# Kernel optimization log

Hardware: AMD Instinct MI355X
Metric: run time of the kernel (lower is better)

## Reference

```python
import jax, jax.numpy as jnp
import numpy as np

E = 8           # ensemble size
D_IN = 512      # input_dim (state+action)
H = 1024        # hidden size, arch=[1024, 1024]
D_OUT = 1       # output_dim (Q value)
LN_EPS = 1e-5


def setup_inputs() -> dict:
    key = jax.random.key(0)
    ks = jax.random.split(key, 8)
    s1 = 1.0 / np.sqrt(D_IN)
    s2 = 1.0 / np.sqrt(H)
    return {
        "x": jax.random.normal(ks[0], (16384, D_IN), dtype=jnp.float32),
        # stacked per-ensemble parameters: leading axis E
        "W1": jax.random.uniform(ks[1], (E, D_IN, H), jnp.float32, -s1, s1),
        "b1": jax.random.uniform(ks[2], (E, H), jnp.float32, -s1, s1),
        "g1": jnp.ones((E, H), jnp.float32),
        "be1": jnp.zeros((E, H), jnp.float32),
        "W2": jax.random.uniform(ks[3], (E, H, H), jnp.float32, -s2, s2),
        "b2": jax.random.uniform(ks[4], (E, H), jnp.float32, -s2, s2),
        "g2": jnp.ones((E, H), jnp.float32),
        "be2": jnp.zeros((E, H), jnp.float32),
        "W3": jax.random.uniform(ks[5], (E, H, D_OUT), jnp.float32, -s2, s2),
        "b3": jax.random.uniform(ks[6], (E, D_OUT), jnp.float32, -s2, s2),
    }


def _layer_norm(h, g, b):
    # h: [E, B, H]; g, b: [E, H] -> broadcast over batch
    mu = jnp.mean(h, axis=-1, keepdims=True)
    var = jnp.mean(jnp.square(h - mu), axis=-1, keepdims=True)
    return (h - mu) * jax.lax.rsqrt(var + LN_EPS) * g[:, None, :] + b[:, None, :]


def reference(x, W1, b1, g1, be1, W2, b2, g2, be2, W3, b3):
    # Layer 1: all ensemble members as one batched GEMM on shared input
    h = jnp.einsum('bd,edh->ebh', x, W1) + b1[:, None, :]       # [E, B, H]
    h = jax.nn.relu(_layer_norm(h, g1, be1))
    # Layer 2
    h = jnp.einsum('ebd,edh->ebh', h, W2) + b2[:, None, :]      # [E, B, H]
    h = jax.nn.relu(_layer_norm(h, g2, be2))
    # Head (identity head activation)
    qs = jnp.einsum('ebd,edo->ebo', h, W3) + b3[:, None, :]      # [E, B, 1]
    q = jnp.min(qs, axis=0)                                      # [B, 1]
    return (q, qs)
```

## Files before the change

kernel.cpp:

```cpp
#include <hip/hip_runtime.h>
#include <hip/hip_bf16.h>
#include <stdint.h>

#define EN    8
#define DIN   512
#define HID   1024
#define BATCH 16384
#define LN_EPS 1e-5f

#define BM 256
#define BN 128
#define BK 32

typedef __bf16   bf16x8 __attribute__((ext_vector_type(8)));
typedef float    f32x4  __attribute__((ext_vector_type(4)));
typedef uint16_t u16x8  __attribute__((ext_vector_type(8)));
typedef uint16_t u16x4  __attribute__((ext_vector_type(4)));
typedef float    fl4    __attribute__((ext_vector_type(4)));

__device__ __forceinline__ uint16_t f2bf(float f) {
  uint32_t x = __builtin_bit_cast(uint32_t, f);
  uint32_t r = (x + 0x7fffu + ((x >> 16) & 1u)) >> 16;
  return (uint16_t)r;
}
__device__ __forceinline__ float bf2f(uint16_t u) {
  return __builtin_bit_cast(float, (uint32_t)u << 16);
}

__device__ __forceinline__ void gload16(const uint16_t* g, uint16_t* lds) {
  __builtin_amdgcn_global_load_lds(
      (const __attribute__((address_space(1))) uint32_t*)g,
      (__attribute__((address_space(3))) uint32_t*)lds, 16, 0, 0);
}

__device__ __forceinline__ f32x4 MF(bf16x8 a, bf16x8 b, f32x4 c) {
  return __builtin_amdgcn_mfma_f32_16x16x32_bf16(a, b, c, 0, 0, 0);
}

__global__ __launch_bounds__(256) void cvt_bf16(const float* __restrict__ src,
                                                uint16_t* __restrict__ dst, long n) {
  long i = ((long)blockIdx.x * 256 + threadIdx.x) * 4;
  if (i >= n) return;
  fl4 v = *(const fl4*)(src + i);
  u16x4 o;
  #pragma unroll
  for (int j = 0; j < 4; ++j) o[j] = f2bf(v[j]);
  *(u16x4*)(dst + i) = o;
}

__global__ __launch_bounds__(256) void transpose_cvt(const float* __restrict__ src,
                                                     uint16_t* __restrict__ dst,
                                                     int R, int C) {
  __shared__ float tile[32][33];
  const int e = blockIdx.z;
  const int c0 = blockIdx.x * 32;
  const int r0 = blockIdx.y * 32;
  const int tx = threadIdx.x & 31, ty = threadIdx.x >> 5;
  const float* s = src + (size_t)e * R * C;
  uint16_t*    d = dst + (size_t)e * R * C;
  #pragma unroll
  for (int i = 0; i < 32; i += 8)
    tile[ty + i][tx] = s[(size_t)(r0 + ty + i) * C + (c0 + tx)];
  __syncthreads();
  #pragma unroll
  for (int i = 0; i < 32; i += 8)
    d[(size_t)(c0 + ty + i) * R + (r0 + tx)] = f2bf(tile[tx][ty + i]);
}

__global__ __launch_bounds__(512, 4) void gemm_rb(
    const uint16_t* __restrict__ A, size_t a_estride,
    const uint16_t* __restrict__ Bt,
    const float*    __restrict__ bias,
    uint16_t*       __restrict__ C,
    int M, int K) {
  __shared__ __attribute__((aligned(16))) char lds[73728];
  const int tid = threadIdx.x;
  const int bx  = blockIdx.x;
  const int e   = bx & 7;
  const int t   = bx >> 3;
  const int mt  = t >> 3;
  const int nt  = t & 7;
  const int NT  = K >> 5;

  const uint16_t* Ae = A + (size_t)e * a_estride + (size_t)(mt * BM) * K;
  const uint16_t* Be = Bt + ((size_t)e * HID + nt * BN) * K;

  const int l  = tid & 63, wid = tid >> 6;
  const int wr = wid >> 1, wc = wid & 1;
  const int fr = l & 15, kq = l >> 4;
  const int swf = (fr ^ (fr >> 2)) & 3;

  const int srow  = tid >> 2;
  const int sunit = (tid & 3) ^ ((srow ^ (srow >> 2)) & 3);
  const uint16_t* pA = Ae + (size_t)srow * K + sunit * 8;
  const uint16_t* pB = Be + (size_t)srow * K + sunit * 8;
  char* const ld_t = lds + tid * 16;

  const int aoff = (wr * 64 + fr) * 64 + ((kq ^ swf) << 4);
  const int boff = 16384 + (wc * 64 + fr) * 64 + ((kq ^ swf) << 4);

  f32x4 acc[4][4];
  #pragma unroll
  for (int i = 0; i < 4; ++i)
    #pragma unroll
    for (int j = 0; j < 4; ++j) acc[i][j] = (f32x4)0.0f;

  auto STAGE = [&](int kt) {
    char* db = ld_t + (kt % 3) * 24576;
    const uint16_t* a0 = pA + kt * BK;
    gload16(a0, (uint16_t*)db);
    gload16(a0 + (size_t)128 * K, (uint16_t*)(db + 8192));
    gload16(pB + kt * BK, (uint16_t*)(db + 16384));
  };

  STAGE(0);
  STAGE(1);
  asm volatile("s_waitcnt vmcnt(3)" ::: "memory");
  __builtin_amdgcn_s_barrier();

  for (int kt = 0; kt < NT; ++kt) {
    if (kt + 2 < NT) STAGE(kt + 2);
    const char* rb = lds + (kt % 3) * 24576;
    bf16x8 af[4], bv[4];
    #pragma unroll
    for (int mi = 0; mi < 4; ++mi) af[mi] = *(const bf16x8*)(rb + aoff + mi * 1024);
    #pragma unroll
    for (int ni = 0; ni < 4; ++ni) bv[ni] = *(const bf16x8*)(rb + boff + ni * 1024);
    __builtin_amdgcn_s_setprio(1);
    #pragma unroll
    for (int ni = 0; ni < 4; ++ni)
      #pragma unroll
      for (int mi = 0; mi < 4; ++mi)
        acc[mi][ni] = MF(af[mi], bv[ni], acc[mi][ni]);
    __builtin_amdgcn_s_setprio(0);
    if (kt + 2 < NT)      asm volatile("s_waitcnt vmcnt(3)" ::: "memory");
    else if (kt + 1 < NT) asm volatile("s_waitcnt vmcnt(0)" ::: "memory");
    if (kt + 1 < NT) __builtin_amdgcn_s_barrier();
  }

  const int col0 = nt * BN + wc * 64 + fr;
  const int row0 = mt * BM + wr * 64 + kq * 4;
  float bvv[4];
  #pragma unroll
  for (int ni = 0; ni < 4; ++ni) bvv[ni] = bias[(size_t)e * HID + col0 + ni * 16];
  #pragma unroll
  for (int mi = 0; mi < 4; ++mi) {
    #pragma unroll
    for (int i = 0; i < 4; ++i) {
      const int rg = row0 + mi * 16 + i;
      uint16_t* cp = C + ((size_t)e * M + rg) * HID + col0;
      #pragma unroll
      for (int ni = 0; ni < 4; ++ni)
        cp[ni * 16] = f2bf(acc[mi][ni][i] + bvv[ni]);
    }
  }
}

__global__ __launch_bounds__(256) void ln_relu(uint16_t* __restrict__ h,
                                               const float* __restrict__ g,
                                               const float* __restrict__ be,
                                               int kshift) {
  const int wid = threadIdx.x >> 6, l = threadIdx.x & 63;
  const long row = (long)blockIdx.x * 4 + wid;
  const int e = (int)(row >> kshift);
  uint16_t* p = h + row * HID;

  u16x8 s0 = *(const u16x8*)(p + l * 8);
  u16x8 s1 = *(const u16x8*)(p + 512 + l * 8);
  float v[16];
  #pragma unroll
  for (int j = 0; j < 8; ++j) { v[j] = bf2f(s0[j]); v[8 + j] = bf2f(s1[j]); }

  float sum = 0.f, sq = 0.f;
  #pragma unroll
  for (int j = 0; j < 16; ++j) { sum += v[j]; sq += v[j] * v[j]; }
  #pragma unroll
  for (int m = 1; m < 64; m <<= 1) {
    sum += __shfl_xor(sum, m);
    sq  += __shfl_xor(sq, m);
  }
  const float mu  = sum * (1.0f / HID);
  const float var = sq * (1.0f / HID) - mu * mu;
  const float rs  = rsqrtf(var + LN_EPS);

  const float* gp = g  + (size_t)e * HID;
  const float* bp = be + (size_t)e * HID;
  u16x8 o0, o1;
  #pragma unroll
  for (int j = 0; j < 8; ++j) {
    const int c0 = l * 8 + j, c1 = 512 + l * 8 + j;
    float x0 = (v[j]     - mu) * rs * gp[c0] + bp[c0];
    float x1 = (v[8 + j] - mu) * rs * gp[c1] + bp[c1];
    o0[j] = f2bf(fmaxf(x0, 0.f));
    o1[j] = f2bf(fmaxf(x1, 0.f));
  }
  *(u16x8*)(p + l * 8) = o0;
  *(u16x8*)(p + 512 + l * 8) = o1;
}

__global__ __launch_bounds__(256) void ln_head(const uint16_t* __restrict__ h,
                                               const float* __restrict__ g,
                                               const float* __restrict__ be,
                                               const float* __restrict__ W3,
                                               const float* __restrict__ b3,
                                               float* __restrict__ out,
                                               int b0, int CB) {
  __shared__ float qsh[EN];
  const int wv = threadIdx.x >> 6, l = threadIdx.x & 63;
  const long b = blockIdx.x;
  #pragma unroll
  for (int ee = 0; ee < 2; ++ee) {
    const int e = wv + ee * 4;
    const uint16_t* p = h + ((size_t)e * CB + b) * HID;
    u16x8 s0 = *(const u16x8*)(p + l * 8);
    u16x8 s1 = *(const u16x8*)(p + 512 + l * 8);
    float v[16];
    #pragma unroll
    for (int j = 0; j < 8; ++j) { v[j] = bf2f(s0[j]); v[8 + j] = bf2f(s1[j]); }
    float sum = 0.f, sq = 0.f;
    #pragma unroll
    for (int j = 0; j < 16; ++j) { sum += v[j]; sq += v[j] * v[j]; }
    #pragma unroll
    for (int m = 1; m < 64; m <<= 1) {
      sum += __shfl_xor(sum, m);
      sq  += __shfl_xor(sq, m);
    }
    const float mu  = sum * (1.0f / HID);
    const float var = sq * (1.0f / HID) - mu * mu;
    const float rs  = rsqrtf(var + LN_EPS);
    const float* gp = g  + (size_t)e * HID;
    const float* bp = be + (size_t)e * HID;
    const float* w  = W3 + (size_t)e * HID;
    float dot = 0.f;
    #pragma unroll
    for (int j = 0; j < 8; ++j) {
      const int c0 = l * 8 + j, c1 = 512 + l * 8 + j;
      float x0 = fmaxf((v[j]     - mu) * rs * gp[c0] + bp[c0], 0.f);
      float x1 = fmaxf((v[8 + j] - mu) * rs * gp[c1] + bp[c1], 0.f);
      dot += x0 * w[c0] + x1 * w[c1];
    }
    #pragma unroll
    for (int m = 1; m < 64; m <<= 1) dot += __shfl_xor(dot, m);
    if (l == 0) {
      const float qe = dot + b3[e];
      qsh[e] = qe;
      out[BATCH + (size_t)e * BATCH + b0 + b] = qe;
    }
  }
  __syncthreads();
  if (threadIdx.x == 0) {
    float m = qsh[0];
    #pragma unroll
    for (int i = 1; i < EN; ++i) m = fminf(m, qsh[i]);
    out[b0 + b] = m;
  }
}

extern "C" void kernel_launch(void* const* d_in, const int* in_sizes, int n_in,
                              void* d_out, int out_size, void* d_ws, size_t ws_size,
                              hipStream_t stream) {
  const float* x   = (const float*)d_in[0];
  const float* W1  = (const float*)d_in[1];
  const float* b1  = (const float*)d_in[2];
  const float* g1  = (const float*)d_in[3];
  const float* be1 = (const float*)d_in[4];
  const float* W2  = (const float*)d_in[5];
  const float* b2  = (const float*)d_in[6];
  const float* g2  = (const float*)d_in[7];
  const float* be2 = (const float*)d_in[8];
  const float* W3  = (const float*)d_in[9];
  const float* b3  = (const float*)d_in[10];
  float* out = (float*)d_out;

  char* ws = (char*)d_ws;
  uint16_t* xb  = (uint16_t*)ws; ws += (size_t)BATCH * DIN * 2;
  uint16_t* w1t = (uint16_t*)ws; ws += (size_t)EN * DIN * HID * 2;
  uint16_t* w2t = (uint16_t*)ws; ws += (size_t)EN * HID * HID * 2;
  size_t fixed = (size_t)(ws - (char*)d_ws);

  size_t avail = (ws_size > fixed) ? (ws_size - fixed) : 0;
  const size_t per_row = 2ULL * EN * HID * 2ULL;
  int CB = BATCH;
  while (CB > 256 && (size_t)CB * per_row > avail) CB >>= 1;
  const int nchunks = BATCH / CB;
  const int kshift = __builtin_ctz(CB);

  uint16_t* h1 = (uint16_t*)ws; ws += (size_t)EN * CB * HID * 2;
  uint16_t* h2 = (uint16_t*)ws;

  cvt_bf16<<<(BATCH * DIN / 4 + 255) / 256, 256, 0, stream>>>(x, xb, (long)BATCH * DIN);
  transpose_cvt<<<dim3(HID / 32, DIN / 32, EN), 256, 0, stream>>>(W1, w1t, DIN, HID);
  transpose_cvt<<<dim3(HID / 32, HID / 32, EN), 256, 0, stream>>>(W2, w2t, HID, HID);

  const int gblocks = (CB / BM) * (HID / BN) * EN;

  for (int c = 0; c < nchunks; ++c) {
    const int b0 = c * CB;
    gemm_rb<<<gblocks, 512, 0, stream>>>(xb + (size_t)b0 * DIN, (size_t)0,
                                         w1t, b1, h1, CB, DIN);
    ln_relu<<<(EN * CB) / 4, 256, 0, stream>>>(h1, g1, be1, kshift);
    gemm_rb<<<gblocks, 512, 0, stream>>>(h1, (size_t)CB * HID,
                                         w2t, b2, h2, CB, HID);
    ln_head<<<CB, 256, 0, stream>>>(h2, g2, be2, W3, b3, out, b0, CB);
  }
}
```

Before: 677.5 us.

## Rewrite GEMM as 256x256 tile, 4-wave kernel with double-buffered LDS

Replaces the 256x128x32 GEMM, which used 8 waves per block and a triple-buffered LDS pipeline, with a 256x256x64 tile computed by 4 waves. Each wave owns a 128x128 sub-tile of 64 accumulators. LDS is double-buffered at 128 KB, with register prefetch of the next k-slice's fragments and an 8-way XOR swizzle. The goal is higher arithmetic intensity per LDS and global byte and fewer barriers. In exchange, each CU runs only one block, which risks register pressure and spills from 256 accumulator VGPRs and gives less latency hiding.

```diff
diff --git a/kernel.cpp b/kernel.cpp
--- a/kernel.cpp
+++ b/kernel.cpp
@@ -8,10 +8,6 @@
 #define BATCH 16384
 #define LN_EPS 1e-5f
 
-#define BM 256
-#define BN 128
-#define BK 32
-
 typedef __bf16   bf16x8 __attribute__((ext_vector_type(8)));
 typedef float    f32x4  __attribute__((ext_vector_type(4)));
 typedef uint16_t u16x8  __attribute__((ext_vector_type(8)));
@@ -27,15 +23,17 @@
   return __builtin_bit_cast(float, (uint32_t)u << 16);
 }
 
-__device__ __forceinline__ void gload16(const uint16_t* g, uint16_t* lds) {
+__device__ __forceinline__ void gload16(const uint16_t* g, char* lds_d) {
   __builtin_amdgcn_global_load_lds(
       (const __attribute__((address_space(1))) uint32_t*)g,
-      (__attribute__((address_space(3))) uint32_t*)lds, 16, 0, 0);
+      (__attribute__((address_space(3))) uint32_t*)lds_d, 16, 0, 0);
 }
 
 __device__ __forceinline__ f32x4 MF(bf16x8 a, bf16x8 b, f32x4 c) {
   return __builtin_amdgcn_mfma_f32_16x16x32_bf16(a, b, c, 0, 0, 0);
 }
+
+#define SB0() __builtin_amdgcn_sched_barrier(0)
 
 __global__ __launch_bounds__(256) void cvt_bf16(const float* __restrict__ src,
                                                 uint16_t* __restrict__ dst, long n) {
@@ -67,91 +65,118 @@
     d[(size_t)(c0 + ty + i) * R + (r0 + tx)] = f2bf(tile[tx][ty + i]);
 }
 
-__global__ __launch_bounds__(512, 4) void gemm_rb(
+__global__ __launch_bounds__(256, 1) void gemm4w(
     const uint16_t* __restrict__ A, size_t a_estride,
     const uint16_t* __restrict__ Bt,
     const float*    __restrict__ bias,
     uint16_t*       __restrict__ C,
     int M, int K) {
-  __shared__ __attribute__((aligned(16))) char lds[73728];
+  __shared__ __attribute__((aligned(16))) char lds[131072];
   const int tid = threadIdx.x;
   const int bx  = blockIdx.x;
   const int e   = bx & 7;
   const int t   = bx >> 3;
-  const int mt  = t >> 3;
-  const int nt  = t & 7;
-  const int NT  = K >> 5;
-
-  const uint16_t* Ae = A + (size_t)e * a_estride + (size_t)(mt * BM) * K;
-  const uint16_t* Be = Bt + ((size_t)e * HID + nt * BN) * K;
+  const int mt  = t >> 2;
+  const int nt  = t & 3;
+  const int NT  = K >> 6;
+
+  const uint16_t* Ae = A + (size_t)e * a_estride + (size_t)(mt * 256) * K;
+  const uint16_t* Be = Bt + ((size_t)e * HID + nt * 256) * K;
 
   const int l  = tid & 63, wid = tid >> 6;
   const int wr = wid >> 1, wc = wid & 1;
-  const int fr = l & 15, kq = l >> 4;
-  const int swf = (fr ^ (fr >> 2)) & 3;
-
-  const int srow  = tid >> 2;
-  const int sunit = (tid & 3) ^ ((srow ^ (srow >> 2)) & 3);
-  const uint16_t* pA = Ae + (size_t)srow * K + sunit * 8;
-  const uint16_t* pB = Be + (size_t)srow * K + sunit * 8;
-  char* const ld_t = lds + tid * 16;
-
-  const int aoff = (wr * 64 + fr) * 64 + ((kq ^ swf) << 4);
-  const int boff = 16384 + (wc * 64 + fr) * 64 + ((kq ^ swf) << 4);
-
-  f32x4 acc[4][4];
-  #pragma unroll
-  for (int i = 0; i < 4; ++i)
-    #pragma unroll
-    for (int j = 0; j < 4; ++j) acc[i][j] = (f32x4)0.0f;
+  const int fr = l & 15, kq = l >> 4, f7 = fr & 7;
+
+  const int r8 = l >> 3;
+  const int su = (l & 7) ^ r8;
+  const uint16_t* pA = Ae + (size_t)(wid * 8 + r8) * K + su * 8;
+  const uint16_t* pB = Be + (size_t)(wid * 8 + r8) * K + su * 8;
+  char* const dst0 = lds + tid * 16;
+
+  const int rdA0 = (wr * 128 + fr) * 128 + ((kq ^ f7) << 4);
+  const int rdB0 = 32768 + (wc * 128 + fr) * 128 + ((kq ^ f7) << 4);
+
+  f32x4 acc[8][8];
+  #pragma unroll
+  for (int i = 0; i < 8; ++i)
+    #pragma unroll
+    for (int j = 0; j < 8; ++j) acc[i][j] = (f32x4)0.0f;
 
   auto STAGE = [&](int kt) {
-    char* db = ld_t + (kt % 3) * 24576;
-    const uint16_t* a0 = pA + kt * BK;
-    gload16(a0, (uint16_t*)db);
-    gload16(a0 + (size_t)128 * K, (uint16_t*)(db + 8192));
-    gload16(pB + kt * BK, (uint16_t*)(db + 16384));
+    char* db = dst0 + ((kt & 1) << 16);
+    const uint16_t* sa = pA + kt * 64;
+    const uint16_t* sb = pB + kt * 64;
+    #pragma unroll
+    for (int j = 0; j < 8; ++j) gload16(sa + (size_t)(j * 32) * K, db + j * 4096);
+    #pragma unroll
+    for (int j = 0; j < 8; ++j) gload16(sb + (size_t)(j * 32) * K, db + 32768 + j * 4096);
   };
 
   STAGE(0);
-  STAGE(1);
-  asm volatile("s_waitcnt vmcnt(3)" ::: "memory");
+  asm volatile("s_waitcnt vmcnt(0)");
+  SB0();
   __builtin_amdgcn_s_barrier();
+  SB0();
+
+  bf16x8 a0[8], b0[8], a1[8], b1[8];
+  {
+    const char* rb = lds;
+    #pragma unroll
+    for (int i = 0; i < 8; ++i) {
+      a0[i] = *(const bf16x8*)(rb + rdA0 + i * 2048);
+      b0[i] = *(const bf16x8*)(rb + rdB0 + i * 2048);
+    }
+  }
 
   for (int kt = 0; kt < NT; ++kt) {
-    if (kt + 2 < NT) STAGE(kt + 2);
-    const char* rb = lds + (kt % 3) * 24576;
-    bf16x8 af[4], bv[4];
-    #pragma unroll
-    for (int mi = 0; mi < 4; ++mi) af[mi] = *(const bf16x8*)(rb + aoff + mi * 1024);
-    #pragma unroll
-    for (int ni = 0; ni < 4; ++ni) bv[ni] = *(const bf16x8*)(rb + boff + ni * 1024);
-    __builtin_amdgcn_s_setprio(1);
-    #pragma unroll
-    for (int ni = 0; ni < 4; ++ni)
+    const char* rb = lds + ((kt & 1) << 16);
+    const char* rq = lds + (((kt + 1) & 1) << 16);
+    if (kt + 1 < NT) STAGE(kt + 1);
+    #pragma unroll
+    for (int mi = 0; mi < 8; ++mi) {
+      a1[mi] = *(const bf16x8*)(rb + ((rdA0 + mi * 2048) ^ 64));
+      b1[mi] = *(const bf16x8*)(rb + ((rdB0 + mi * 2048) ^ 64));
+      __builtin_amdgcn_s_setprio(1);
       #pragma unroll
-      for (int mi = 0; mi < 4; ++mi)
-        acc[mi][ni] = MF(af[mi], bv[ni], acc[mi][ni]);
-    __builtin_amdgcn_s_setprio(0);
-    if (kt + 2 < NT)      asm volatile("s_waitcnt vmcnt(3)" ::: "memory");
-    else if (kt + 1 < NT) asm volatile("s_waitcnt vmcnt(0)" ::: "memory");
-    if (kt + 1 < NT) __builtin_amdgcn_s_barrier();
-  }
-
-  const int col0 = nt * BN + wc * 64 + fr;
-  const int row0 = mt * BM + wr * 64 + kq * 4;
-  float bvv[4];
-  #pragma unroll
-  for (int ni = 0; ni < 4; ++ni) bvv[ni] = bias[(size_t)e * HID + col0 + ni * 16];
-  #pragma unroll
-  for (int mi = 0; mi < 4; ++mi) {
+      for (int ni = 0; ni < 8; ++ni)
+        acc[mi][ni] = MF(a0[mi], b0[ni], acc[mi][ni]);
+      __builtin_amdgcn_s_setprio(0);
+    }
+    #pragma unroll
+    for (int mi = 0; mi < 8; ++mi) {
+      __builtin_amdgcn_s_setprio(1);
+      #pragma unroll
+      for (int ni = 0; ni < 8; ++ni)
+        acc[mi][ni] = MF(a1[mi], b1[ni], acc[mi][ni]);
+      __builtin_amdgcn_s_setprio(0);
+    }
+    if (kt + 1 < NT) {
+      asm volatile("s_waitcnt vmcnt(0)");
+      SB0();
+      __builtin_amdgcn_s_barrier();
+      SB0();
+      #pragma unroll
+      for (int i = 0; i < 8; ++i) {
+        a0[i] = *(const bf16x8*)(rq + rdA0 + i * 2048);
+        b0[i] = *(const bf16x8*)(rq + rdB0 + i * 2048);
+      }
+    }
+  }
+
+  const int col0 = nt * 256 + wc * 128 + fr;
+  const int row0 = mt * 256 + wr * 128 + kq * 4;
+  float bv[8];
+  #pragma unroll
+  for (int ni = 0; ni < 8; ++ni) bv[ni] = bias[(size_t)e * HID + col0 + ni * 16];
+  #pragma unroll
+  for (int mi = 0; mi < 8; ++mi) {
     #pragma unroll
     for (int i = 0; i < 4; ++i) {
       const int rg = row0 + mi * 16 + i;
       uint16_t* cp = C + ((size_t)e * M + rg) * HID + col0;
       #pragma unroll
-      for (int ni = 0; ni < 4; ++ni)
-        cp[ni * 16] = f2bf(acc[mi][ni][i] + bvv[ni]);
+      for (int ni = 0; ni < 8; ++ni)
+        cp[ni * 16] = f2bf(acc[mi][ni][i] + bv[ni]);
     }
   }
 }
@@ -292,15 +317,15 @@
   transpose_cvt<<<dim3(HID / 32, DIN / 32, EN), 256, 0, stream>>>(W1, w1t, DIN, HID);
   transpose_cvt<<<dim3(HID / 32, HID / 32, EN), 256, 0, stream>>>(W2, w2t, HID, HID);
 
-  const int gblocks = (CB / BM) * (HID / BN) * EN;
+  const int gblocks = (CB / 256) * (HID / 256) * EN;
 
   for (int c = 0; c < nchunks; ++c) {
     const int b0 = c * CB;
-    gemm_rb<<<gblocks, 512, 0, stream>>>(xb + (size_t)b0 * DIN, (size_t)0,
-                                         w1t, b1, h1, CB, DIN);
+    gemm4w<<<gblocks, 256, 0, stream>>>(xb + (size_t)b0 * DIN, (size_t)0,
+                                        w1t, b1, h1, CB, DIN);
     ln_relu<<<(EN * CB) / 4, 256, 0, stream>>>(h1, g1, be1, kshift);
-    gemm_rb<<<gblocks, 512, 0, stream>>>(h1, (size_t)CB * HID,
-                                         w2t, b2, h2, CB, HID);
+    gemm4w<<<gblocks, 256, 0, stream>>>(h1, (size_t)CB * HID,
+                                        w2t, b2, h2, CB, HID);
     ln_head<<<CB, 256, 0, stream>>>(h2, g2, be2, W3, b3, out, b0, CB);
   }
 }
```

Result: faster. 659.8 us (median of 4 runs) (-2.6%).

## Use 256-thread GEMM blocks with 128x64 per-warp tiles and new LDS swizzle

Applied to the files above, without the earlier changes.

The GEMM kernel drops from 512 to 256 threads per block while keeping the 256x128 block tile, so each wave now computes a 128x64 sub-tile with 8x4 MFMA accumulators. This doubles register-level reuse of the B fragments per LDS read. The LDS layout and swizzle change to 128-byte rows with a new XOR pattern, and each thread issues six async global-to-LDS loads per stage. The s_setprio hints are removed, and the doubled accumulator set raises register pressure, lowering occupancy to two blocks per CU.

```diff
diff --git a/kernel.cpp b/kernel.cpp
--- a/kernel.cpp
+++ b/kernel.cpp
@@ -8,10 +8,6 @@
 #define BATCH 16384
 #define LN_EPS 1e-5f
 
-#define BM 256
-#define BN 128
-#define BK 32
-
 typedef __bf16   bf16x8 __attribute__((ext_vector_type(8)));
 typedef float    f32x4  __attribute__((ext_vector_type(4)));
 typedef uint16_t u16x8  __attribute__((ext_vector_type(8)));
@@ -27,10 +23,10 @@
   return __builtin_bit_cast(float, (uint32_t)u << 16);
 }
 
-__device__ __forceinline__ void gload16(const uint16_t* g, uint16_t* lds) {
+__device__ __forceinline__ void gload16(const uint16_t* g, char* lds_d) {
   __builtin_amdgcn_global_load_lds(
       (const __attribute__((address_space(1))) uint32_t*)g,
-      (__attribute__((address_space(3))) uint32_t*)lds, 16, 0, 0);
+      (__attribute__((address_space(3))) uint32_t*)lds_d, 16, 0, 0);
 }
 
 __device__ __forceinline__ f32x4 MF(bf16x8 a, bf16x8 b, f32x4 c) {
@@ -67,7 +63,7 @@
     d[(size_t)(c0 + ty + i) * R + (r0 + tx)] = f2bf(tile[tx][ty + i]);
 }
 
-__global__ __launch_bounds__(512, 4) void gemm_rb(
+__global__ __launch_bounds__(256, 2) void gemm_t2(
     const uint16_t* __restrict__ A, size_t a_estride,
     const uint16_t* __restrict__ Bt,
     const float*    __restrict__ bias,
@@ -82,69 +78,76 @@
   const int nt  = t & 7;
   const int NT  = K >> 5;
 
-  const uint16_t* Ae = A + (size_t)e * a_estride + (size_t)(mt * BM) * K;
-  const uint16_t* Be = Bt + ((size_t)e * HID + nt * BN) * K;
+  const uint16_t* Ae = A + (size_t)e * a_estride + (size_t)(mt * 256) * K;
+  const uint16_t* Be = Bt + ((size_t)e * HID + nt * 128) * K;
 
   const int l  = tid & 63, wid = tid >> 6;
   const int wr = wid >> 1, wc = wid & 1;
   const int fr = l & 15, kq = l >> 4;
-  const int swf = (fr ^ (fr >> 2)) & 3;
-
-  const int srow  = tid >> 2;
-  const int sunit = (tid & 3) ^ ((srow ^ (srow >> 2)) & 3);
-  const uint16_t* pA = Ae + (size_t)srow * K + sunit * 8;
-  const uint16_t* pB = Be + (size_t)srow * K + sunit * 8;
-  char* const ld_t = lds + tid * 16;
-
-  const int aoff = (wr * 64 + fr) * 64 + ((kq ^ swf) << 4);
-  const int boff = 16384 + (wc * 64 + fr) * 64 + ((kq ^ swf) << 4);
-
-  f32x4 acc[4][4];
-  #pragma unroll
-  for (int i = 0; i < 4; ++i)
+
+  const int pl = (tid >> 3) & 7;
+  const int su = (tid & 7) ^ pl;
+  const int r0 = 2 * (tid >> 3) + (su >> 2);
+  const int j8 = (su & 3) * 8;
+  const uint16_t* pA = Ae + (size_t)r0 * K + j8;
+  const uint16_t* pB = Be + (size_t)r0 * K + j8;
+  char* const ldst = lds + tid * 16;
+
+  const int un   = (((fr & 1) << 2) | kq) ^ (fr >> 1);
+  const int aoff = (wr * 64 + (fr >> 1)) * 128 + un * 16;
+  const int boff = 16384 + (wc * 32 + (fr >> 1)) * 128 + un * 16;
+
+  f32x4 acc[8][4];
+  #pragma unroll
+  for (int i = 0; i < 8; ++i)
     #pragma unroll
     for (int j = 0; j < 4; ++j) acc[i][j] = (f32x4)0.0f;
 
-  auto STAGE = [&](int kt) {
-    char* db = ld_t + (kt % 3) * 24576;
-    const uint16_t* a0 = pA + kt * BK;
-    gload16(a0, (uint16_t*)db);
-    gload16(a0 + (size_t)128 * K, (uint16_t*)(db + 8192));
-    gload16(pB + kt * BK, (uint16_t*)(db + 16384));
+  auto STAGE = [&](int kt, int slot) {
+    char* db = ldst + slot * 24576;
+    const uint16_t* sa = pA + kt * 32;
+    const uint16_t* sb = pB + kt * 32;
+    #pragma unroll
+    for (int c = 0; c < 4; ++c) gload16(sa + (size_t)(c * 64) * K, db + c * 4096);
+    #pragma unroll
+    for (int c = 0; c < 2; ++c) gload16(sb + (size_t)(c * 64) * K, db + 16384 + c * 4096);
   };
 
-  STAGE(0);
-  STAGE(1);
-  asm volatile("s_waitcnt vmcnt(3)" ::: "memory");
+  STAGE(0, 0);
+  STAGE(1, 1);
+  asm volatile("s_waitcnt vmcnt(6)");
   __builtin_amdgcn_s_barrier();
 
+  int scur = 0;
   for (int kt = 0; kt < NT; ++kt) {
-    if (kt + 2 < NT) STAGE(kt + 2);
-    const char* rb = lds + (kt % 3) * 24576;
-    bf16x8 af[4], bv[4];
-    #pragma unroll
-    for (int mi = 0; mi < 4; ++mi) af[mi] = *(const bf16x8*)(rb + aoff + mi * 1024);
+    if (kt + 2 < NT) {
+      int s2 = scur + 2; if (s2 >= 3) s2 -= 3;
+      STAGE(kt + 2, s2);
+    }
+    const char* rb = lds + scur * 24576;
+    bf16x8 af[8], bv[4];
+    #pragma unroll
+    for (int mi = 0; mi < 8; ++mi) af[mi] = *(const bf16x8*)(rb + aoff + mi * 1024);
     #pragma unroll
     for (int ni = 0; ni < 4; ++ni) bv[ni] = *(const bf16x8*)(rb + boff + ni * 1024);
-    __builtin_amdgcn_s_setprio(1);
-    #pragma unroll
-    for (int ni = 0; ni < 4; ++ni)
+    #pragma unroll
+    for (int mi = 0; mi < 8; ++mi)
       #pragma unroll
-      for (int mi = 0; mi < 4; ++mi)
+      for (int ni = 0; ni < 4; ++ni)
         acc[mi][ni] = MF(af[mi], bv[ni], acc[mi][ni]);
-    __builtin_amdgcn_s_setprio(0);
-    if (kt + 2 < NT)      asm volatile("s_waitcnt vmcnt(3)" ::: "memory");
-    else if (kt + 1 < NT) asm volatile("s_waitcnt vmcnt(0)" ::: "memory");
+    if (kt + 2 < NT)      asm volatile("s_waitcnt vmcnt(6)");
+    else if (kt + 1 < NT) asm volatile("s_waitcnt vmcnt(0)");
     if (kt + 1 < NT) __builtin_amdgcn_s_barrier();
-  }
-
-  const int col0 = nt * BN + wc * 64 + fr;
-  const int row0 = mt * BM + wr * 64 + kq * 4;
+    scur = (scur + 1 == 3) ? 0 : scur + 1;
+  }
+
+  const int col0 = nt * 128 + wc * 64 + fr;
+  const int row0 = mt * 256 + wr * 128 + kq * 4;
   float bvv[4];
   #pragma unroll
   for (int ni = 0; ni < 4; ++ni) bvv[ni] = bias[(size_t)e * HID + col0 + ni * 16];
   #pragma unroll
-  for (int mi = 0; mi < 4; ++mi) {
+  for (int mi = 0; mi < 8; ++mi) {
     #pragma unroll
     for (int i = 0; i < 4; ++i) {
       const int rg = row0 + mi * 16 + i;
@@ -292,14 +295,14 @@
   transpose_cvt<<<dim3(HID / 32, DIN / 32, EN), 256, 0, stream>>>(W1, w1t, DIN, HID);
   transpose_cvt<<<dim3(HID / 32, HID / 32, EN), 256, 0, stream>>>(W2, w2t, HID, HID);
 
-  const int gblocks = (CB / BM) * (HID / BN) * EN;
+  const int gblocks = (CB / 256) * (HID / 128) * EN;
 
   for (int c = 0; c < nchunks; ++c) {
     const int b0 = c * CB;
-    gemm_rb<<<gblocks, 512, 0, stream>>>(xb + (size_t)b0 * DIN, (size_t)0,
+    gemm_t2<<<gblocks, 256, 0, stream>>>(xb + (size_t)b0 * DIN, (size_t)0,
                                          w1t, b1, h1, CB, DIN);
     ln_relu<<<(EN * CB) / 4, 256, 0, stream>>>(h1, g1, be1, kshift);
-    gemm_rb<<<gblocks, 512, 0, stream>>>(h1, (size_t)CB * HID,
+    gemm_t2<<<gblocks, 256, 0, stream>>>(h1, (size_t)CB * HID,
                                          w2t, b2, h2, CB, HID);
     ln_head<<<CB, 256, 0, stream>>>(h2, g2, be2, W3, b3, out, b0, CB);
   }
```

Result: no change. 670.9 us (-1.0%).
